# Optimization experiments

Measured on AMD Instinct MI355X. Metric: run time of the kernel, lower is better.

The kernel has to match this reference:

```python
import jax, jax.numpy as jnp
import numpy as np

D_MODEL = 1024
N_HEADS = 16


def setup_inputs() -> dict:
    key = jax.random.key(0)
    ks = jax.random.split(key, 11)
    B, L, D = 2, 2048, D_MODEL
    s = 1.0 / np.sqrt(D)
    return {
        "q": jax.random.normal(ks[0], (B, L, D), jnp.float32),
        "k": jax.random.normal(ks[1], (B, L, D), jnp.float32),
        "v": jax.random.normal(ks[2], (B, L, D), jnp.float32),
        "w_q": jax.random.normal(ks[3], (D, D), jnp.float32) * s,
        "b_q": jnp.zeros((D,), jnp.float32),
        "w_k": jax.random.normal(ks[4], (D, D), jnp.float32) * s,
        "b_k": jnp.zeros((D,), jnp.float32),
        "w_v": jax.random.normal(ks[5], (D, D), jnp.float32) * s,
        "b_v": jnp.zeros((D,), jnp.float32),
        "w_o": jax.random.normal(ks[6], (D, D), jnp.float32) * s,
        "b_o": jnp.zeros((D,), jnp.float32),
    }


def reference(q, k, v, w_q, b_q, w_k, b_k, w_v, b_v, w_o, b_o):
    B, L, D = q.shape
    H = N_HEADS
    d_h = D // H
    # QKV projections (nn.Linear: x @ W^T + b)
    qh = (q @ w_q.T + b_q).reshape(B, L, H, d_h).transpose(0, 2, 1, 3)  # [B,H,L,d_h]
    kh = (k @ w_k.T + b_k).reshape(B, L, H, d_h).transpose(0, 2, 1, 3)
    vh = (v @ w_v.T + b_v).reshape(B, L, H, d_h).transpose(0, 2, 1, 3)
    # scaled dot-product attention
    scores = jnp.einsum('bhqd,bhkd->bhqk', qh, kh) / jnp.sqrt(jnp.float32(d_h))
    attn = jax.nn.softmax(scores, axis=-1)                               # [B,H,L,L]
    ctx = jnp.einsum('bhqk,bhkd->bhqd', attn, vh)                        # [B,H,L,d_h]
    ctx = ctx.transpose(0, 2, 1, 3).reshape(B, L, D)
    out = ctx @ w_o.T + b_o
    return out, attn
```

## Files before the change

kernel.cpp:

```cpp
#include <hip/hip_runtime.h>
#include <hip/hip_bf16.h>
#include <stdint.h>

#define DEV static __device__ __forceinline__

typedef float f32x4 __attribute__((ext_vector_type(4)));
typedef __bf16 bf16x8 __attribute__((ext_vector_type(8)));
typedef unsigned short u16x8 __attribute__((ext_vector_type(8)));
typedef unsigned short u16x4 __attribute__((ext_vector_type(4)));
typedef uint32_t u32x4 __attribute__((ext_vector_type(4)));
typedef unsigned short u16;

#define B_ 2
#define L_ 2048
#define D_MODEL_ 1024
#define H_ 16
#define DH_ 64

#define SHIFT2 11.5415603f

DEV u16 f2bf(float f) {
  union { float f; uint32_t u; } v; v.f = f;
  uint32_t r = v.u + 0x7FFFu + ((v.u >> 16) & 1u);
  return (u16)(r >> 16);
}

DEV float exp2v(float x) {
#if __has_builtin(__builtin_amdgcn_exp2f)
  return __builtin_amdgcn_exp2f(x);
#else
  float r;
  asm("v_exp_f32 %0, %1" : "=v"(r) : "v"(x));
  return r;
#endif
}

DEV uint32_t pkbf(float a, float b) {
  __hip_bfloat162 h = __float22bfloat162_rn(float2{a, b});
  union { __hip_bfloat162 h; uint32_t u; } cv; cv.h = h;
  return cv.u;
}

DEV f32x4 mfma16(bf16x8 a, bf16x8 b, f32x4 c) {
  return __builtin_amdgcn_mfma_f32_16x16x32_bf16(a, b, c, 0, 0, 0);
}

DEV void gl_lds16(const void* g, void* l) {
  __builtin_amdgcn_global_load_lds(
      (const __attribute__((address_space(1))) unsigned int*)g,
      (__attribute__((address_space(3))) unsigned int*)l, 16, 0, 0);
}

struct CastArgs {
  const float* src[8];
  u16* dst[8];
  int n8[8];
};

__global__ __launch_bounds__(256) void cast_kernel(CastArgs a) {
  const int z = blockIdx.z;
  u16* d = a.dst[z];
  const int n8 = a.n8[z];
  const int stride = gridDim.x * blockDim.x;
  const float* s = a.src[z];
  if (s == nullptr) {
    for (int i = blockIdx.x * blockDim.x + threadIdx.x; i < n8; i += stride)
      *((u16x8*)d + i) = u16x8{0, 0, 0, 0, 0, 0, 0, 0};
    return;
  }
  for (int i = blockIdx.x * blockDim.x + threadIdx.x; i < n8; i += stride) {
    const float4* sp = (const float4*)s + (size_t)i * 2;
    float4 x0 = sp[0], x1 = sp[1];
    u16x8 o;
    o[0] = f2bf(x0.x); o[1] = f2bf(x0.y); o[2] = f2bf(x0.z); o[3] = f2bf(x0.w);
    o[4] = f2bf(x1.x); o[5] = f2bf(x1.y); o[6] = f2bf(x1.z); o[7] = f2bf(x1.w);
    *((u16x8*)d + i) = o;
  }
}

#define GM 4096
#define GN 1024
#define GK 1024

struct GemmArgs {
  const u16* X[3];
  const u16* W[3];
  const float* bias[3];
  void* out[3];
  float alpha[3];
  int mode[3];
};

__global__ __launch_bounds__(256) void gemm_bt(GemmArgs g) {
  const int z = blockIdx.z;
  const u16* X = g.X[z];
  const u16* W = g.W[z];
  const float* bias = g.bias[z];
  const float alpha = g.alpha[z];
  const int mode = g.mode[z];
  const int m0 = blockIdx.y * 128, n0 = blockIdx.x * 128;

  __shared__ __align__(16) char smem[32 * 1024];
  char* As = smem;
  char* Bs = smem + 16 * 1024;

  const int tid = threadIdx.x;
  const int lane = tid & 63, w = tid >> 6;
  const int l15 = lane & 15, l4 = lane >> 4;
  const int wm = (w >> 1) * 64, wn = (w & 1) * 64;

  f32x4 acc[4][4];
#pragma unroll
  for (int i = 0; i < 4; ++i)
#pragma unroll
    for (int j = 0; j < 4; ++j) acc[i][j] = f32x4{0.f, 0.f, 0.f, 0.f};

  for (int ks = 0; ks < GK; ks += 64) {
    __syncthreads();
    for (int c = w; c < 16; c += 4) {
      int r = c * 8 + (lane >> 3);
      int j = lane & 7;
      int sj = j ^ (r & 7);
      gl_lds16((const char*)(X + (size_t)(m0 + r) * GK + ks) + sj * 16, As + c * 1024);
      gl_lds16((const char*)(W + (size_t)(n0 + r) * GK + ks) + sj * 16, Bs + c * 1024);
    }
    __syncthreads();
#pragma unroll
    for (int ksub = 0; ksub < 2; ++ksub) {
      bf16x8 af[4], bfr[4];
#pragma unroll
      for (int mf = 0; mf < 4; ++mf) {
        int r = wm + mf * 16 + l15;
        int j16 = ksub * 4 + l4;
        af[mf] = *(const bf16x8*)(As + r * 128 + ((j16 ^ (r & 7)) * 16));
      }
#pragma unroll
      for (int nf = 0; nf < 4; ++nf) {
        int r = wn + nf * 16 + l15;
        int j16 = ksub * 4 + l4;
        bfr[nf] = *(const bf16x8*)(Bs + r * 128 + ((j16 ^ (r & 7)) * 16));
      }
#pragma unroll
      for (int mf = 0; mf < 4; ++mf)
#pragma unroll
        for (int nf = 0; nf < 4; ++nf) acc[mf][nf] = mfma16(af[mf], bfr[nf], acc[mf][nf]);
    }
  }

  if (mode == 2) {
    u16* base = (u16*)g.out[z];
#pragma unroll
    for (int nf = 0; nf < 4; ++nf) {
      int n = n0 + wn + nf * 16 + l15;
      float bv = bias[n];
      int df = (n & 63) >> 4, fl15 = n & 15, hh = n >> 6;
#pragma unroll
      for (int mf = 0; mf < 4; ++mf) {
        int m = m0 + wm + mf * 16 + l4 * 4;
        u16x4 pk;
#pragma unroll
        for (int r = 0; r < 4; ++r) pk[r] = f2bf((acc[mf][nf][r] + bv) * alpha);
        int lg = m & 2047, bb = m >> 11;
        int t = lg >> 6, lc = lg & 63;
        int c = lc >> 3, e = lc & 7;
        size_t off = ((((size_t)(bb * H_ + hh) * 32 + t) * 8 + (c >> 2) * 4 + df) * 512) +
                     ((c & 3) * 16 + fl15) * 8 + e;
        *(u16x4*)(base + off) = pk;
      }
    }
  } else {
#pragma unroll
    for (int nf = 0; nf < 4; ++nf) {
      int n = n0 + wn + nf * 16 + l15;
      float bv = bias[n];
#pragma unroll
      for (int mf = 0; mf < 4; ++mf) {
#pragma unroll
        for (int r = 0; r < 4; ++r) {
          int m = m0 + wm + mf * 16 + l4 * 4 + r;
          float val = (acc[mf][nf][r] + bv) * alpha;
          if (mode == 1)
            ((float*)g.out[z])[(size_t)m * GN + n] = val;
          else
            ((u16*)g.out[z])[(size_t)m * GN + n] = f2bf(val);
        }
      }
    }
  }
}

__global__ __launch_bounds__(256) void sumexp_kernel(const u16* Qp, const u16* Kp,
                                                     float* sums) {
  const int q0 = blockIdx.x * 64;
  const int kc0 = blockIdx.y * 512;
  const int bh = blockIdx.z;
  const int b = bh >> 4, h = bh & 15;
  const int tid = threadIdx.x, lane = tid & 63, w = tid >> 6;
  const int l15 = lane & 15, l4 = lane >> 4;
  const int lr = lane >> 3, lj = lane & 7;

  __shared__ __align__(16) char smem[16 * 1024];

  const u16* Qbase = Qp + ((size_t)(b * L_ + q0 + w * 16) * D_MODEL_ + h * DH_);
  const u16* Kbase = Kp + ((size_t)(b * L_ + kc0) * D_MODEL_ + h * DH_);

  auto stK = [&](int t) {
    const int c0 = t * 64, bsel = (t & 1) << 13;
    for (int c = w; c < 8; c += 4) {
      int r = c * 8 + lr, sj = lj ^ (r & 7);
      gl_lds16((const char*)(Kbase + (size_t)(c0 + r) * D_MODEL_) + sj * 16,
               smem + bsel + c * 1024);
    }
  };

  bf16x8 qa[2];
#pragma unroll
  for (int ksub = 0; ksub < 2; ++ksub)
    qa[ksub] = *(const bf16x8*)(Qbase + (size_t)l15 * D_MODEL_ + (ksub * 4 + l4) * 8);

  stK(0);
  __syncthreads();

  float ssum = 0.f;
  for (int t = 0; t < 8; ++t) {
    if (t < 7) stK(t + 1);
    const char* Ks = smem + ((t & 1) << 13);
    f32x4 s[4];
#pragma unroll
    for (int nf = 0; nf < 4; ++nf) s[nf] = f32x4{0.f, 0.f, 0.f, 0.f};
#pragma unroll
    for (int ksub = 0; ksub < 2; ++ksub) {
      int j16 = ksub * 4 + l4;
      bf16x8 kb[4];
#pragma unroll
      for (int nf = 0; nf < 4; ++nf) {
        int r = nf * 16 + l15;
        kb[nf] = *(const bf16x8*)(Ks + r * 128 + ((j16 ^ (r & 7)) * 16));
      }
#pragma unroll
      for (int nf = 0; nf < 4; ++nf) s[nf] = mfma16(kb[nf], qa[ksub], s[nf]);
    }
#pragma unroll
    for (int nf = 0; nf < 4; ++nf)
#pragma unroll
      for (int r = 0; r < 4; ++r) ssum += exp2v(s[nf][r] - SHIFT2);
    __syncthreads();
  }

  ssum += __shfl_xor(ssum, 16);
  ssum += __shfl_xor(ssum, 32);
  if (lane < 16)
    atomicAdd(&sums[((size_t)bh << 11) + q0 + w * 16 + lane], ssum);
}

__global__ __launch_bounds__(256) void attn_kernel(const u16* Qp, const u16* Kp,
                                                   const u16* VF, const float* sums,
                                                   float* attn, u16* ctx) {
  const int bid = blockIdx.x;
  const int lid = (bid & 7) * 128 + (bid >> 3);
  const int q0 = (lid & 31) * 64;
  const int h = (lid >> 5) & 15;
  const int b = lid >> 9;
  const int tid = threadIdx.x, lane = tid & 63, w = tid >> 6;
  const int l15 = lane & 15, l4 = lane >> 4;
  const int lr = lane >> 3, lj = lane & 7;

  __shared__ __align__(16) char smem[32 * 1024];
  char* Pw = smem + w * 4096;

  const u16* Qbase = Qp + ((size_t)(b * L_ + q0 + w * 16) * D_MODEL_ + h * DH_);
  const u16* Kbase = Kp + ((size_t)(b * L_) * D_MODEL_ + h * DH_);
  const u16* Vb = VF + ((size_t)(b * H_ + h) * 32) * 4096;
  float* attnb = attn + ((size_t)(b * H_ + h)) * L_ * L_;

  auto stK = [&](int t) {
    const int c0 = t * 64, bsel = (t & 1) << 13;
    for (int c = w; c < 8; c += 4) {
      int r = c * 8 + lr, sj = lj ^ (r & 7);
      gl_lds16((const char*)(Kbase + (size_t)(c0 + r) * D_MODEL_) + sj * 16,
               smem + 16384 + bsel + c * 1024);
    }
  };

  bf16x8 qa[2];
#pragma unroll
  for (int ksub = 0; ksub < 2; ++ksub)
    qa[ksub] = *(const bf16x8*)(Qbase + (size_t)l15 * D_MODEL_ + (ksub * 4 + l4) * 8);

  const float c2 =
      SHIFT2 + __log2f(sums[(((size_t)(b * H_ + h)) << 11) + q0 + w * 16 + l15]);

  stK(0);

  f32x4 cacc[4];
#pragma unroll
  for (int i = 0; i < 4; ++i) cacc[i] = f32x4{0.f, 0.f, 0.f, 0.f};

  const int swz = l15 & 7;
  float* awave = attnb + (size_t)(q0 + w * 16) * L_;
  __syncthreads();

  for (int t = 0; t < 32; ++t) {
    const int c0 = t * 64;
    if (t < 31) stK(t + 1);
    const u16* Vt = Vb + (size_t)t * 4096;
    bf16x8 va[2][4];
#pragma unroll
    for (int ksub = 0; ksub < 2; ++ksub)
#pragma unroll
      for (int df = 0; df < 4; ++df)
        va[ksub][df] = *(const bf16x8*)(Vt + (ksub * 4 + df) * 512 + lane * 8);
    __builtin_amdgcn_sched_barrier(0);

    const char* Ks = smem + 16384 + ((t & 1) << 13);
    f32x4 s[4];
#pragma unroll
    for (int nf = 0; nf < 4; ++nf) s[nf] = f32x4{0.f, 0.f, 0.f, 0.f};
    __builtin_amdgcn_s_setprio(1);
#pragma unroll
    for (int ksub = 0; ksub < 2; ++ksub) {
      int j16 = ksub * 4 + l4;
      bf16x8 kb[4];
#pragma unroll
      for (int nf = 0; nf < 4; ++nf) {
        int r = nf * 16 + l15;
        kb[nf] = *(const bf16x8*)(Ks + r * 128 + ((j16 ^ (r & 7)) * 16));
      }
#pragma unroll
      for (int nf = 0; nf < 4; ++nf) s[nf] = mfma16(kb[nf], qa[ksub], s[nf]);
    }
    __builtin_amdgcn_s_setprio(0);

#pragma unroll
    for (int nf = 0; nf < 4; ++nf) {
      f32x4 p4;
#pragma unroll
      for (int r = 0; r < 4; ++r) p4[r] = exp2v(s[nf][r] - c2);
      *(f32x4*)(Pw + l15 * 256 + (((nf * 4 + l4) ^ swz) * 16)) = p4;
    }
#pragma unroll
    for (int j = 0; j < 4; ++j) {
      int row = 4 * j + (lane >> 4);
      f32x4 v = *(const f32x4*)(Pw + row * 256 + (((lane & 15) ^ (row & 7)) * 16));
      __builtin_nontemporal_store(
          v, (f32x4*)(awave + (size_t)row * L_ + c0 + (lane & 15) * 4));
    }
    __builtin_amdgcn_s_setprio(1);
#pragma unroll
    for (int ksub = 0; ksub < 2; ++ksub) {
      int cbase = (ksub * 4 + l4) * 2;
      f32x4 plo = *(const f32x4*)(Pw + l15 * 256 + ((cbase ^ swz) * 16));
      f32x4 phi = *(const f32x4*)(Pw + l15 * 256 + (((cbase + 1) ^ swz) * 16));
      union { u32x4 u; bf16x8 h; } pa;
      pa.u[0] = pkbf(plo[0], plo[1]);
      pa.u[1] = pkbf(plo[2], plo[3]);
      pa.u[2] = pkbf(phi[0], phi[1]);
      pa.u[3] = pkbf(phi[2], phi[3]);
#pragma unroll
      for (int df = 0; df < 4; ++df)
        cacc[df] = mfma16(pa.h, va[ksub][df], cacc[df]);
    }
    __builtin_amdgcn_s_setprio(0);
    if (t < 31) {
      asm volatile("s_waitcnt vmcnt(12)" ::: "memory");
      __builtin_amdgcn_s_barrier();
      __builtin_amdgcn_sched_barrier(0);
    }
  }

#pragma unroll
  for (int df = 0; df < 4; ++df) {
#pragma unroll
    for (int r = 0; r < 4; ++r) {
      int row = q0 + w * 16 + l4 * 4 + r;
      int col = h * DH_ + df * 16 + l15;
      ctx[(size_t)(b * L_ + row) * D_MODEL_ + col] = f2bf(cacc[df][r]);
    }
  }
}

extern "C" void kernel_launch(void* const* d_in, const int* in_sizes, int n_in,
                              void* d_out, int out_size, void* d_ws, size_t ws_size,
                              hipStream_t stream) {
  const float* q = (const float*)d_in[0];
  const float* k = (const float*)d_in[1];
  const float* v = (const float*)d_in[2];
  const float* w_q = (const float*)d_in[3];
  const float* b_q = (const float*)d_in[4];
  const float* w_k = (const float*)d_in[5];
  const float* b_k = (const float*)d_in[6];
  const float* w_v = (const float*)d_in[7];
  const float* b_v = (const float*)d_in[8];
  const float* w_o = (const float*)d_in[9];
  const float* b_o = (const float*)d_in[10];

  float* out = (float*)d_out;
  float* attn = (float*)d_out + (size_t)B_ * L_ * D_MODEL_;

  const size_t MB = 1u << 20;
  char* ws = (char*)d_ws;
  u16* qb = (u16*)(ws + 0 * MB);
  u16* kb = (u16*)(ws + 8 * MB);
  u16* vb = (u16*)(ws + 16 * MB);
  u16* wqb = (u16*)(ws + 24 * MB);
  u16* wkb = (u16*)(ws + 26 * MB);
  u16* wvb = (u16*)(ws + 28 * MB);
  u16* wob = (u16*)(ws + 30 * MB);
  u16* Qp = (u16*)(ws + 32 * MB);
  u16* Kp = (u16*)(ws + 40 * MB);
  u16* VF = (u16*)(ws + 48 * MB);
  float* sums = (float*)(ws + 56 * MB);
  u16* ctx = kb;

  CastArgs ca;
  ca.src[0] = q;   ca.dst[0] = qb;  ca.n8[0] = (B_ * L_ * D_MODEL_) / 8;
  ca.src[1] = k;   ca.dst[1] = kb;  ca.n8[1] = (B_ * L_ * D_MODEL_) / 8;
  ca.src[2] = v;   ca.dst[2] = vb;  ca.n8[2] = (B_ * L_ * D_MODEL_) / 8;
  ca.src[3] = w_q; ca.dst[3] = wqb; ca.n8[3] = (D_MODEL_ * D_MODEL_) / 8;
  ca.src[4] = w_k; ca.dst[4] = wkb; ca.n8[4] = (D_MODEL_ * D_MODEL_) / 8;
  ca.src[5] = w_v; ca.dst[5] = wvb; ca.n8[5] = (D_MODEL_ * D_MODEL_) / 8;
  ca.src[6] = w_o; ca.dst[6] = wob; ca.n8[6] = (D_MODEL_ * D_MODEL_) / 8;
  ca.src[7] = nullptr; ca.dst[7] = (u16*)sums; ca.n8[7] = (B_ * H_ * L_ * 4) / 16;
  cast_kernel<<<dim3(1024, 1, 8), 256, 0, stream>>>(ca);

  GemmArgs ga;
  ga.X[0] = qb;  ga.W[0] = wqb; ga.bias[0] = b_q; ga.out[0] = Qp; ga.alpha[0] = 0.125f * 1.44269504f; ga.mode[0] = 0;
  ga.X[1] = kb;  ga.W[1] = wkb; ga.bias[1] = b_k; ga.out[1] = Kp; ga.alpha[1] = 1.f;    ga.mode[1] = 0;
  ga.X[2] = vb;  ga.W[2] = wvb; ga.bias[2] = b_v; ga.out[2] = VF; ga.alpha[2] = 1.f;    ga.mode[2] = 2;
  gemm_bt<<<dim3(8, 32, 3), 256, 0, stream>>>(ga);

  sumexp_kernel<<<dim3(32, 4, 32), 256, 0, stream>>>(Qp, Kp, sums);

  attn_kernel<<<dim3(1024, 1, 1), 256, 0, stream>>>(Qp, Kp, VF, sums, attn, ctx);

  GemmArgs go;
  go.X[0] = ctx; go.W[0] = wob; go.bias[0] = b_o; go.out[0] = out; go.alpha[0] = 1.f; go.mode[0] = 1;
  go.X[1] = ctx; go.W[1] = wob; go.bias[1] = b_o; go.out[1] = out; go.alpha[1] = 1.f; go.mode[1] = 1;
  go.X[2] = ctx; go.W[2] = wob; go.bias[2] = b_o; go.out[2] = out; go.alpha[2] = 1.f; go.mode[2] = 1;
  gemm_bt<<<dim3(8, 32, 1), 256, 0, stream>>>(go);
}
```

Measured before the change: 245.8 us.

## Store K projection in MFMA fragment layout and load directly to registers

```diff
diff --git a/kernel.cpp b/kernel.cpp
--- a/kernel.cpp
+++ b/kernel.cpp
@@ -168,6 +168,28 @@
         *(u16x4*)(base + off) = pk;
       }
     }
+  } else if (mode == 3) {
+    u16* base = (u16*)g.out[z];
+#pragma unroll
+    for (int nf = 0; nf < 4; ++nf) {
+      int n = n0 + wn + nf * 16 + l15;
+      float bv = bias[n];
+      int dh = n & 63, hh = n >> 6;
+      int c = dh >> 3;
+      int fragb = (c >> 2) * 4, laneb = (c & 3) * 16, e = dh & 7;
+#pragma unroll
+      for (int mf = 0; mf < 4; ++mf) {
+#pragma unroll
+        for (int r = 0; r < 4; ++r) {
+          int m = m0 + wm + mf * 16 + l4 * 4 + r;
+          int lg = m & 2047, bb = m >> 11;
+          int t = lg >> 6, nfk = (lg >> 4) & 3, l15k = lg & 15;
+          size_t off = ((((size_t)(bb * H_ + hh) * 32 + t) * 8 + fragb + nfk) * 512) +
+                       (laneb + l15k) * 8 + e;
+          base[off] = f2bf((acc[mf][nf][r] + bv) * alpha);
+        }
+      }
+    }
   } else {
 #pragma unroll
     for (int nf = 0; nf < 4; ++nf) {
@@ -189,62 +211,44 @@
   }
 }
 
-__global__ __launch_bounds__(256) void sumexp_kernel(const u16* Qp, const u16* Kp,
+__global__ __launch_bounds__(256) void sumexp_kernel(const u16* Qp, const u16* KF,
                                                      float* sums) {
   const int q0 = blockIdx.x * 64;
-  const int kc0 = blockIdx.y * 512;
+  const int tb = blockIdx.y * 8;
   const int bh = blockIdx.z;
   const int b = bh >> 4, h = bh & 15;
   const int tid = threadIdx.x, lane = tid & 63, w = tid >> 6;
   const int l15 = lane & 15, l4 = lane >> 4;
-  const int lr = lane >> 3, lj = lane & 7;
-
-  __shared__ __align__(16) char smem[16 * 1024];
 
   const u16* Qbase = Qp + ((size_t)(b * L_ + q0 + w * 16) * D_MODEL_ + h * DH_);
-  const u16* Kbase = Kp + ((size_t)(b * L_ + kc0) * D_MODEL_ + h * DH_);
-
-  auto stK = [&](int t) {
-    const int c0 = t * 64, bsel = (t & 1) << 13;
-    for (int c = w; c < 8; c += 4) {
-      int r = c * 8 + lr, sj = lj ^ (r & 7);
-      gl_lds16((const char*)(Kbase + (size_t)(c0 + r) * D_MODEL_) + sj * 16,
-               smem + bsel + c * 1024);
-    }
-  };
+  const u16* Kf = KF + ((size_t)bh * 32) * 4096;
 
   bf16x8 qa[2];
 #pragma unroll
   for (int ksub = 0; ksub < 2; ++ksub)
     qa[ksub] = *(const bf16x8*)(Qbase + (size_t)l15 * D_MODEL_ + (ksub * 4 + l4) * 8);
 
-  stK(0);
-  __syncthreads();
-
   float ssum = 0.f;
   for (int t = 0; t < 8; ++t) {
-    if (t < 7) stK(t + 1);
-    const char* Ks = smem + ((t & 1) << 13);
+    const u16* Kt = Kf + (size_t)(tb + t) * 4096;
     f32x4 s[4];
 #pragma unroll
     for (int nf = 0; nf < 4; ++nf) s[nf] = f32x4{0.f, 0.f, 0.f, 0.f};
+    __builtin_amdgcn_s_setprio(1);
 #pragma unroll
     for (int ksub = 0; ksub < 2; ++ksub) {
-      int j16 = ksub * 4 + l4;
       bf16x8 kb[4];
 #pragma unroll
-      for (int nf = 0; nf < 4; ++nf) {
-        int r = nf * 16 + l15;
-        kb[nf] = *(const bf16x8*)(Ks + r * 128 + ((j16 ^ (r & 7)) * 16));
-      }
+      for (int nf = 0; nf < 4; ++nf)
+        kb[nf] = *(const bf16x8*)(Kt + (ksub * 4 + nf) * 512 + lane * 8);
 #pragma unroll
       for (int nf = 0; nf < 4; ++nf) s[nf] = mfma16(kb[nf], qa[ksub], s[nf]);
     }
+    __builtin_amdgcn_s_setprio(0);
 #pragma unroll
     for (int nf = 0; nf < 4; ++nf)
 #pragma unroll
       for (int r = 0; r < 4; ++r) ssum += exp2v(s[nf][r] - SHIFT2);
-    __syncthreads();
   }
 
   ssum += __shfl_xor(ssum, 16);
@@ -253,7 +257,7 @@
     atomicAdd(&sums[((size_t)bh << 11) + q0 + w * 16 + lane], ssum);
 }
 
-__global__ __launch_bounds__(256) void attn_kernel(const u16* Qp, const u16* Kp,
+__global__ __launch_bounds__(256) void attn_kernel(const u16* Qp, const u16* KF,
                                                    const u16* VF, const float* sums,
                                                    float* attn, u16* ctx) {
   const int bid = blockIdx.x;
@@ -263,25 +267,15 @@
   const int b = lid >> 9;
   const int tid = threadIdx.x, lane = tid & 63, w = tid >> 6;
   const int l15 = lane & 15, l4 = lane >> 4;
-  const int lr = lane >> 3, lj = lane & 7;
-
-  __shared__ __align__(16) char smem[32 * 1024];
+
+  __shared__ __align__(16) char smem[16 * 1024];
   char* Pw = smem + w * 4096;
 
   const u16* Qbase = Qp + ((size_t)(b * L_ + q0 + w * 16) * D_MODEL_ + h * DH_);
-  const u16* Kbase = Kp + ((size_t)(b * L_) * D_MODEL_ + h * DH_);
+  const u16* Kf = KF + ((size_t)(b * H_ + h) * 32) * 4096;
   const u16* Vb = VF + ((size_t)(b * H_ + h) * 32) * 4096;
   float* attnb = attn + ((size_t)(b * H_ + h)) * L_ * L_;
 
-  auto stK = [&](int t) {
-    const int c0 = t * 64, bsel = (t & 1) << 13;
-    for (int c = w; c < 8; c += 4) {
-      int r = c * 8 + lr, sj = lj ^ (r & 7);
-      gl_lds16((const char*)(Kbase + (size_t)(c0 + r) * D_MODEL_) + sj * 16,
-               smem + 16384 + bsel + c * 1024);
-    }
-  };
-
   bf16x8 qa[2];
 #pragma unroll
   for (int ksub = 0; ksub < 2; ++ksub)
@@ -290,45 +284,34 @@
   const float c2 =
       SHIFT2 + __log2f(sums[(((size_t)(b * H_ + h)) << 11) + q0 + w * 16 + l15]);
 
-  stK(0);
-
   f32x4 cacc[4];
 #pragma unroll
   for (int i = 0; i < 4; ++i) cacc[i] = f32x4{0.f, 0.f, 0.f, 0.f};
 
   const int swz = l15 & 7;
   float* awave = attnb + (size_t)(q0 + w * 16) * L_;
-  __syncthreads();
 
   for (int t = 0; t < 32; ++t) {
     const int c0 = t * 64;
-    if (t < 31) stK(t + 1);
+    const u16* Kt = Kf + (size_t)t * 4096;
     const u16* Vt = Vb + (size_t)t * 4096;
-    bf16x8 va[2][4];
+    bf16x8 kb[2][4], va[2][4];
 #pragma unroll
     for (int ksub = 0; ksub < 2; ++ksub)
 #pragma unroll
-      for (int df = 0; df < 4; ++df)
-        va[ksub][df] = *(const bf16x8*)(Vt + (ksub * 4 + df) * 512 + lane * 8);
-    __builtin_amdgcn_sched_barrier(0);
-
-    const char* Ks = smem + 16384 + ((t & 1) << 13);
+      for (int i = 0; i < 4; ++i) {
+        kb[ksub][i] = *(const bf16x8*)(Kt + (ksub * 4 + i) * 512 + lane * 8);
+        va[ksub][i] = *(const bf16x8*)(Vt + (ksub * 4 + i) * 512 + lane * 8);
+      }
+
     f32x4 s[4];
 #pragma unroll
     for (int nf = 0; nf < 4; ++nf) s[nf] = f32x4{0.f, 0.f, 0.f, 0.f};
     __builtin_amdgcn_s_setprio(1);
 #pragma unroll
-    for (int ksub = 0; ksub < 2; ++ksub) {
-      int j16 = ksub * 4 + l4;
-      bf16x8 kb[4];
-#pragma unroll
-      for (int nf = 0; nf < 4; ++nf) {
-        int r = nf * 16 + l15;
-        kb[nf] = *(const bf16x8*)(Ks + r * 128 + ((j16 ^ (r & 7)) * 16));
-      }
-#pragma unroll
-      for (int nf = 0; nf < 4; ++nf) s[nf] = mfma16(kb[nf], qa[ksub], s[nf]);
-    }
+    for (int ksub = 0; ksub < 2; ++ksub)
+#pragma unroll
+      for (int nf = 0; nf < 4; ++nf) s[nf] = mfma16(kb[ksub][nf], qa[ksub], s[nf]);
     __builtin_amdgcn_s_setprio(0);
 
 #pragma unroll
@@ -361,11 +344,6 @@
         cacc[df] = mfma16(pa.h, va[ksub][df], cacc[df]);
     }
     __builtin_amdgcn_s_setprio(0);
-    if (t < 31) {
-      asm volatile("s_waitcnt vmcnt(12)" ::: "memory");
-      __builtin_amdgcn_s_barrier();
-      __builtin_amdgcn_sched_barrier(0);
-    }
   }
 
 #pragma unroll
@@ -407,7 +385,7 @@
   u16* wvb = (u16*)(ws + 28 * MB);
   u16* wob = (u16*)(ws + 30 * MB);
   u16* Qp = (u16*)(ws + 32 * MB);
-  u16* Kp = (u16*)(ws + 40 * MB);
+  u16* KF = (u16*)(ws + 40 * MB);
   u16* VF = (u16*)(ws + 48 * MB);
   float* sums = (float*)(ws + 56 * MB);
   u16* ctx = kb;
@@ -425,13 +403,13 @@
 
   GemmArgs ga;
   ga.X[0] = qb;  ga.W[0] = wqb; ga.bias[0] = b_q; ga.out[0] = Qp; ga.alpha[0] = 0.125f * 1.44269504f; ga.mode[0] = 0;
-  ga.X[1] = kb;  ga.W[1] = wkb; ga.bias[1] = b_k; ga.out[1] = Kp; ga.alpha[1] = 1.f;    ga.mode[1] = 0;
+  ga.X[1] = kb;  ga.W[1] = wkb; ga.bias[1] = b_k; ga.out[1] = KF; ga.alpha[1] = 1.f;    ga.mode[1] = 3;
   ga.X[2] = vb;  ga.W[2] = wvb; ga.bias[2] = b_v; ga.out[2] = VF; ga.alpha[2] = 1.f;    ga.mode[2] = 2;
   gemm_bt<<<dim3(8, 32, 3), 256, 0, stream>>>(ga);
 
-  sumexp_kernel<<<dim3(32, 4, 32), 256, 0, stream>>>(Qp, Kp, sums);
-
-  attn_kernel<<<dim3(1024, 1, 1), 256, 0, stream>>>(Qp, Kp, VF, sums, attn, ctx);
+  sumexp_kernel<<<dim3(32, 4, 32), 256, 0, stream>>>(Qp, KF, sums);
+
+  attn_kernel<<<dim3(1024, 1, 1), 256, 0, stream>>>(Qp, KF, VF, sums, attn, ctx);
 
   GemmArgs go;
   go.X[0] = ctx; go.W[0] = wob; go.bias[0] = b_o; go.out[0] = out; go.alpha[0] = 1.f; go.mode[0] = 1;
```

Result: no change. 241.8 us (-1.6%).
